# Kernel optimization log

Hardware: AMD Instinct MI355X
Metric: run time of the kernel (lower is better)

## Reference

```python
import jax, jax.numpy as jnp
import numpy as np

D_MODEL = 768
HEADS = 12
D_HEAD = D_MODEL // HEADS
D_DYNA = 768
EPS = 1e-5
B, SP, SI = 16, 256, 1024


def _layernorm(x, g, b):
    mu = jnp.mean(x, axis=-1, keepdims=True)
    var = jnp.var(x, axis=-1, keepdims=True)
    return (x - mu) * jax.lax.rsqrt(var + EPS) * g + b


def _mha(q, k, v, wq, bq, wk, bk, wv, bv, wo, bo):
    # weights stored [d_in, d_out]; torch Linear math y = x @ W^T + b is
    # equivalent with transposed storage.
    B_ = q.shape[0]
    qh = (q @ wq + bq).reshape(B_, -1, HEADS, D_HEAD)
    kh = (k @ wk + bk).reshape(B_, -1, HEADS, D_HEAD)
    vh = (v @ wv + bv).reshape(B_, -1, HEADS, D_HEAD)
    scores = jnp.einsum('bqhd,bkhd->bhqk', qh, kh) / np.sqrt(D_HEAD).astype(np.float32)
    attn = jax.nn.softmax(scores, axis=-1)  # dropout disabled (eval)
    out = jnp.einsum('bhqk,bkhd->bqhd', attn, vh).reshape(B_, -1, D_MODEL)
    return out @ wo + bo


def setup_inputs() -> dict:
    key = jax.random.key(0)
    ks = iter(jax.random.split(key, 40))
    s = 0.02
    d = {
        'image': jax.random.normal(next(ks), (B, SI, D_MODEL), jnp.float32),
        'prompt': jax.random.normal(next(ks), (B, SP, D_MODEL), jnp.float32),
        'posi': jax.random.normal(next(ks), (B, SI, D_MODEL), jnp.float32),
        'posp': jax.random.normal(next(ks), (B, SP, D_MODEL), jnp.float32),
    }
    for ln in ('ln_p1', 'ln_p2', 'ln_p3', 'ln_i1'):
        d[ln + '_g'] = jnp.ones((D_MODEL,), jnp.float32)
        d[ln + '_b'] = jnp.zeros((D_MODEL,), jnp.float32)
    for pre in ('pp', 'pi'):
        for nm in ('q', 'k', 'v', 'o'):
            d[f'{pre}_w{nm}'] = s * jax.random.normal(next(ks), (D_MODEL, D_MODEL), jnp.float32)
            d[f'{pre}_b{nm}'] = jnp.zeros((D_MODEL,), jnp.float32)
    d['ff_w1'] = s * jax.random.normal(next(ks), (D_MODEL, D_MODEL), jnp.float32)
    d['ff_b1'] = jnp.zeros((D_MODEL,), jnp.float32)
    d['ff_w2'] = s * jax.random.normal(next(ks), (D_MODEL, D_DYNA), jnp.float32)
    d['ff_b2'] = jnp.zeros((D_DYNA,), jnp.float32)
    return d


def reference(image, prompt, posi, posp,
              ln_p1_g, ln_p1_b, ln_p2_g, ln_p2_b, ln_p3_g, ln_p3_b, ln_i1_g, ln_i1_b,
              pp_wq, pp_bq, pp_wk, pp_bk, pp_wv, pp_bv, pp_wo, pp_bo,
              pi_wq, pi_bq, pi_wk, pi_bk, pi_wv, pi_bv, pi_wo, pi_bo,
              ff_w1, ff_b1, ff_w2, ff_b2):
    prompt0 = prompt + posp
    xp = _layernorm(prompt0, ln_p1_g, ln_p1_b)
    xp = _mha(xp, xp, xp, pp_wq, pp_bq, pp_wk, pp_bk, pp_wv, pp_bv, pp_wo, pp_bo)
    prompt = prompt + xp  # dropout_p1 is identity in eval
    xp = _layernorm(prompt + prompt0, ln_p2_g, ln_p2_b)
    xi = _layernorm(image + posi, ln_i1_g, ln_i1_b)
    xp = _mha(xp, xi, xi, pi_wq, pi_bq, pi_wk, pi_bk, pi_wv, pi_bv, pi_wo, pi_bo)
    prompt = prompt + xp  # dropout_p2 identity
    xp = _layernorm(prompt + prompt0, ln_p3_g, ln_p3_b)
    xp = jax.nn.relu(xp @ ff_w1 + ff_b1) @ ff_w2 + ff_b2
    return xp
```

## Files before the change

### kernel.cpp

```cpp
#include <hip/hip_runtime.h>
#include <hip/hip_bf16.h>
#include <stdint.h>
#include <math.h>

#define D_MODEL 768
#define HEADS 12
#define D_HEAD 64
#define BATCH 16
#define SP 256
#define SI 1024
#define NP (BATCH * SP)
#define NI (BATCH * SI)

#define GLOBAL_AS __attribute__((address_space(1)))
#define LDS_AS    __attribute__((address_space(3)))

typedef __attribute__((ext_vector_type(8))) short  frag_ab;
typedef __attribute__((ext_vector_type(4))) float  frag_cd;

static __device__ __forceinline__ ushort f2bf(float f) {
  __hip_bfloat16 h = __float2bfloat16(f);
  return *(ushort*)&h;
}
static __device__ __forceinline__ float bf2f(ushort u) {
  return __bfloat162float(*(__hip_bfloat16*)&u);
}
static __device__ __forceinline__ bool probe_bf(const uint32_t* p) {
  return p[0] == 0x3F803F80u;
}

struct Prep {
  const void* wsrc[10]; ushort* wdst[10];
  const void* vsrc[18]; float* vdst;
};

__global__ __launch_bounds__(256) void prep_kernel(Prep p, const uint32_t* probe) {
  const bool isbf = probe_bf(probe);
  const int z = blockIdx.z;
  if (z < 10) {
    __shared__ float tile[32][33];
    const int tx = threadIdx.x & 31, ty = threadIdx.x >> 5;
    const int x0 = blockIdx.x * 32, y0 = blockIdx.y * 32;
    const void* src = p.wsrc[z];
    ushort* dst = p.wdst[z];
#pragma unroll
    for (int i = 0; i < 4; i++) {
      const int y = y0 + ty + i * 8;
      float v;
      if (isbf) v = bf2f(((const ushort*)src)[(size_t)y * 768 + x0 + tx]);
      else      v = ((const float*)src)[(size_t)y * 768 + x0 + tx];
      tile[ty + i * 8][tx] = v;
    }
    __syncthreads();
#pragma unroll
    for (int i = 0; i < 4; i++) {
      const int row = x0 + ty + i * 8;
      const int col = y0 + tx;
      dst[(size_t)row * 768 + col] = f2bf(tile[tx][ty + i * 8]);
    }
  } else {
    const int idx = (blockIdx.y * 24 + blockIdx.x) * 256 + threadIdx.x;
    if (idx < 18 * 768) {
      const int e = idx / 768, i = idx - e * 768;
      float v;
      if (isbf) v = bf2f(((const ushort*)p.vsrc[e])[i]);
      else      v = ((const float*)p.vsrc[e])[i];
      p.vdst[idx] = v;
    }
  }
}

struct LNJob {
  const void* a; const void* b;
  const float* g; const float* be;
  float* sum_out; ushort* ln_out;
  int nrows; int abf;
};

__global__ __launch_bounds__(192) void add_ln2(LNJob J0, LNJob J1, const uint32_t* probe) {
  int row = blockIdx.x;
  LNJob j = (row < J0.nrows) ? J0 : J1;
  if (row >= J0.nrows) row -= J0.nrows;
  const int tid = threadIdx.x;
  const size_t base = (size_t)row * D_MODEL;
  const int c0 = tid * 4;
  const bool isbf = j.abf && probe_bf(probe);
  float x[4];
  if (isbf) {
    const uint2 ua = *(const uint2*)((const ushort*)j.a + base + c0);
    const uint2 ub = *(const uint2*)((const ushort*)j.b + base + c0);
    const ushort* pa = (const ushort*)&ua;
    const ushort* pb = (const ushort*)&ub;
#pragma unroll
    for (int t = 0; t < 4; t++) x[t] = bf2f(pa[t]) + bf2f(pb[t]);
  } else {
    const float4 fa = *(const float4*)((const float*)j.a + base + c0);
    const float4 fb = *(const float4*)((const float*)j.b + base + c0);
    x[0] = fa.x + fb.x; x[1] = fa.y + fb.y; x[2] = fa.z + fb.z; x[3] = fa.w + fb.w;
  }
  if (j.sum_out) {
    float4 s4; s4.x = x[0]; s4.y = x[1]; s4.z = x[2]; s4.w = x[3];
    *(float4*)&j.sum_out[base + c0] = s4;
  }
  __shared__ float rs[192], rq[192];
  __shared__ float stats[2];
  rs[tid] = x[0] + x[1] + x[2] + x[3];
  rq[tid] = x[0]*x[0] + x[1]*x[1] + x[2]*x[2] + x[3]*x[3];
  __syncthreads();
  if (tid < 64) {
    float s = rs[tid] + rs[tid + 64] + rs[tid + 128];
    float q = rq[tid] + rq[tid + 64] + rq[tid + 128];
#pragma unroll
    for (int o = 32; o > 0; o >>= 1) { s += __shfl_down(s, o); q += __shfl_down(q, o); }
    if (tid == 0) {
      const float mu  = s * (1.0f / D_MODEL);
      const float var = q * (1.0f / D_MODEL) - mu * mu;
      stats[0] = mu;
      stats[1] = rsqrtf(var + 1e-5f);
    }
  }
  __syncthreads();
  const float mu = stats[0], inv = stats[1];
  const float4 gv = *(const float4*)&j.g[c0];
  const float4 bv = *(const float4*)&j.be[c0];
  uint2 ou;
  ushort* oe = (ushort*)&ou;
  oe[0] = f2bf((x[0] - mu) * inv * gv.x + bv.x);
  oe[1] = f2bf((x[1] - mu) * inv * gv.y + bv.y);
  oe[2] = f2bf((x[2] - mu) * inv * gv.z + bv.z);
  oe[3] = f2bf((x[3] - mu) * inv * gv.w + bv.w);
  *(uint2*)(j.ln_out + base + c0) = ou;
}

#define BAR   __builtin_amdgcn_s_barrier()
#define LGKM0 do { asm volatile("s_waitcnt lgkmcnt(0)" ::: "memory"); \
                   __builtin_amdgcn_sched_barrier(0); } while (0)
#define VMC4  do { asm volatile("s_waitcnt vmcnt(4)" ::: "memory"); \
                   __builtin_amdgcn_sched_barrier(0); } while (0)

#define RD_A(SL) do { \
  const ushort* _b = &lds[SL][0][0]; \
  _Pragma("unroll") for (int _m = 0; _m < 4; ++_m) \
  _Pragma("unroll") for (int _k = 0; _k < 2; ++_k) \
    aF[_m][_k] = *(const frag_ab*)(_b + ((wr << 6) + _m * 16 + ml) * 64 + \
                                   (((_k << 5) + (kq << 3)) ^ swz)); \
} while (0)

#define RD_B(DST, SL, no) do { \
  const ushort* _b = &lds[SL][1][0]; \
  _Pragma("unroll") for (int _n = 0; _n < 2; ++_n) \
  _Pragma("unroll") for (int _k = 0; _k < 2; ++_k) \
    DST[_n][_k] = *(const frag_ab*)(_b + ((wc << 6) + (no) + _n * 16 + ml) * 64 + \
                                    (((_k << 5) + (kq << 3)) ^ swz)); \
} while (0)

#define MM(NB, BF) do { \
  __builtin_amdgcn_s_setprio(1); \
  _Pragma("unroll") for (int _m = 0; _m < 4; ++_m) \
  _Pragma("unroll") for (int _n = 0; _n < 2; ++_n) \
  _Pragma("unroll") for (int _k = 0; _k < 2; ++_k) \
    acc[_m][(NB) + _n] = __builtin_amdgcn_mfma_f32_16x16x32_bf16( \
        aF[_m][_k], BF[_n][_k], acc[_m][(NB) + _n], 0, 0, 0); \
  __builtin_amdgcn_s_setprio(0); \
} while (0)

#define STAGE(SL, RG, PTR, RBASE, KT) do { \
  const ushort* _p = (PTR) + (size_t)((RBASE) + srow) * 768 + ((KT) << 6) + scol; \
  _Pragma("unroll") for (int _j = 0; _j < 4; ++_j) \
    __builtin_amdgcn_global_load_lds( \
        (const GLOBAL_AS void*)(_p + (size_t)(_j * 32) * 768), \
        (LDS_AS void*)((LDS_AS ushort*)&lds[SL][RG][0] + (((_j << 2) + w) << 9)), \
        16, 0, 0); \
} while (0)

#define ENGINE128() do { \
  STAGE(0, 0, jA, m0, 0); \
  STAGE(0, 1, jB, n0, 0); \
  STAGE(1, 0, jA, m0, 1); \
  VMC4; BAR; \
  for (int it = 0; it < 6; ++it) { \
    const int t1  = 2 * it + 1; \
    const int tn0 = (2 * it + 2 < 12) ? 2 * it + 2 : 11; \
    const int tn1 = (2 * it + 3 < 12) ? 2 * it + 3 : 11; \
    RD_A(0); RD_B(bF0, 0, 0); \
    STAGE(1, 1, jB, n0, t1); \
    BAR; LGKM0; \
    MM(0, bF0); \
    BAR; \
    RD_B(bF1, 0, 32); \
    STAGE(0, 0, jA, m0, tn0); \
    BAR; LGKM0; \
    MM(2, bF1); \
    VMC4; BAR; \
    RD_A(1); RD_B(bF0, 1, 0); \
    STAGE(0, 1, jB, n0, tn0); \
    BAR; LGKM0; \
    MM(0, bF0); \
    BAR; \
    RD_B(bF1, 1, 32); \
    STAGE(1, 0, jA, m0, tn1); \
    BAR; LGKM0; \
    MM(2, bF1); \
    VMC4; BAR; \
  } \
} while (0)

struct GJob {
  const ushort* A; const ushort* Bt; const float* bias;
  ushort* o0; ushort* o1; ushort* vT;
  int X; int vsub; int shift;
};

__global__ __launch_bounds__(256, 2) void gemm_mega128(GJob J0, GJob J1, int n0blocks) {
  __shared__ __align__(16) ushort lds[2][2][8192];
  int bid = blockIdx.x;
  GJob j = (bid < n0blocks) ? J0 : J1;
  if (bid >= n0blocks) bid -= n0blocks;
  const int tid  = threadIdx.x;
  const int lane = tid & 63, w = tid >> 6;
  const int wr = w >> 1, wc = w & 1;
  const int ml = lane & 15, kq = lane >> 4;
  const int rest = bid >> 3;
  const int x = rest % j.X, y = (bid & 7) + 8 * (rest / j.X);
  const int m0 = y << 7, n0 = x << 7;
  const int srow = (w << 3) + (lane >> 3);
  const int scol = (((lane & 7) ^ (lane >> 3)) << 3);
  const int swz  = (ml & 7) << 3;
  const ushort* jA = j.A;
  const ushort* jB = j.Bt;

  frag_cd acc[4][4] = {};
  frag_ab aF[4][2], bF0[2][2], bF1[2][2];

  ENGINE128();

  const int sub  = x / 6;
  const int mask = (1 << j.shift) - 1;
#pragma unroll
  for (int mt = 0; mt < 4; mt++) {
#pragma unroll
    for (int nt = 0; nt < 4; nt++) {
      const int row0 = m0 + wr * 64 + mt * 16 + kq * 4;
      const int col  = n0 + wc * 64 + nt * 16 + ml;
      const float bc = j.bias[col];
      if (sub == j.vsub) {
        const int hcol = col - sub * 768;
        const int hh = hcol >> 6, dd = hcol & 63;
        const int bb = row0 >> j.shift;
        const int jj = row0 & mask;
        uint2 pack;
        ushort* pe = (ushort*)&pack;
#pragma unroll
        for (int r = 0; r < 4; r++) pe[r] = f2bf(acc[mt][nt][r] + bc);
        *(uint2*)(j.vT + ((((size_t)(bb * HEADS + hh) << 6) + dd) << j.shift) + jj) = pack;
      } else {
        ushort* out = (sub == 0) ? j.o0 : j.o1;
        const int cl = col - sub * 768;
#pragma unroll
        for (int r = 0; r < 4; r++)
          out[(size_t)(row0 + r) * 768 + cl] = f2bf(acc[mt][nt][r] + bc);
      }
    }
  }
}

__global__ __launch_bounds__(256, 2) void gemm_v3(
    const ushort* __restrict__ A, const ushort* __restrict__ Bt,
    const float* __restrict__ bias,
    const void* __restrict__ resid, int rmode,
    void* __restrict__ C, int relu, int omode,
    const uint32_t* __restrict__ probe, int X) {
  __shared__ __align__(16) ushort lds[2][2][8192];
  const int bid = blockIdx.x;
  const int tid  = threadIdx.x;
  const int lane = tid & 63, w = tid >> 6;
  const int wr = w >> 1, wc = w & 1;
  const int ml = lane & 15, kq = lane >> 4;
  const int rest = bid >> 3;
  const int x = rest % X, y = (bid & 7) + 8 * (rest / X);
  const int m0 = y << 7, n0 = x << 7;
  const int srow = (w << 3) + (lane >> 3);
  const int scol = (((lane & 7) ^ (lane >> 3)) << 3);
  const int swz  = (ml & 7) << 3;
  const ushort* jA = A;
  const ushort* jB = Bt;

  frag_cd acc[4][4] = {};
  frag_ab aF[4][2], bF0[2][2], bF1[2][2];

  ENGINE128();

  const bool obf = (omode == 1) || (omode == 2 && probe_bf(probe));
  const bool rbf = (rmode == 2) && probe_bf(probe);
#pragma unroll
  for (int mt = 0; mt < 4; mt++) {
#pragma unroll
    for (int nt = 0; nt < 4; nt++) {
      const int row0 = m0 + wr * 64 + mt * 16 + kq * 4;
      const int col  = n0 + wc * 64 + nt * 16 + ml;
      const float bc = bias[col];
#pragma unroll
      for (int r = 0; r < 4; r++) {
        const size_t off = (size_t)(row0 + r) * 768 + col;
        float v = acc[mt][nt][r] + bc;
        if (rmode != 0)
          v += rbf ? bf2f(((const ushort*)resid)[off]) : ((const float*)resid)[off];
        if (relu) v = fmaxf(v, 0.f);
        if (obf) ((ushort*)C)[off] = f2bf(v);
        else     ((float*)C)[off]  = v;
      }
    }
  }
}

#undef RD_A
#undef RD_B
#undef MM
#undef STAGE
#undef ENGINE128

#define FS 68
__global__ __launch_bounds__(256) void fattn_mfma(
    const ushort* __restrict__ Q, const ushort* __restrict__ Kp,
    const ushort* __restrict__ vT, ushort* __restrict__ O, int Skv) {
  __shared__ __align__(16) ushort Qs[64 * FS];
  __shared__ __align__(16) ushort Ks[64 * FS];
  __shared__ __align__(16) ushort Vt[64 * FS];
  __shared__ __align__(16) ushort Ps[64 * FS];
  const int tid  = threadIdx.x;
  const int lane = tid & 63, w = tid >> 6;
  const int ml   = lane & 15, kq = lane >> 4;
  const int bid = blockIdx.x;
  const int g8  = bid & 7;
  const int qt  = (bid >> 3) & 3;
  const int g   = (bid >> 5) * 8 + g8;
  const int h   = g % HEADS;
  const int b   = g / HEADS;
  const int q0  = qt * 64;
  const ushort* Qb  = Q  + ((size_t)b * SP + q0) * D_MODEL + h * D_HEAD;
  const ushort* Kb  = Kp + (size_t)b * Skv * D_MODEL + h * D_HEAD;
  const ushort* vTb = vT + (size_t)g * 64 * Skv;

  const int r0 = tid >> 3, p0 = tid & 7;
  const int r1 = r0 + 32;

  for (int c = tid; c < 512; c += 256) {
    const int r = c >> 3, p = c & 7;
    *(uint4*)&Qs[r * FS + p * 8] = *(const uint4*)(Qb + (size_t)r * D_MODEL + p * 8);
  }
  __syncthreads();
  frag_ab qa[2];
#pragma unroll
  for (int kc = 0; kc < 2; kc++)
    qa[kc] = *(const frag_ab*)&Qs[(w * 16 + ml) * FS + kc * 32 + kq * 8];

  frag_cd oc[4] = {};
  float m_i[4], l_i[4];
#pragma unroll
  for (int r = 0; r < 4; r++) { m_i[r] = -1e30f; l_i[r] = 0.f; }
  const float SCL = 0.125f * 1.44269504f;

  uint4 kr0 = *(const uint4*)(Kb + (size_t)r0 * D_MODEL + p0 * 8);
  uint4 vr0 = *(const uint4*)(vTb + (size_t)r0 * Skv + p0 * 8);
  uint4 kr1 = *(const uint4*)(Kb + (size_t)r1 * D_MODEL + p0 * 8);
  uint4 vr1 = *(const uint4*)(vTb + (size_t)r1 * Skv + p0 * 8);

  for (int j0 = 0; j0 < Skv; j0 += 64) {
    __syncthreads();
    *(uint4*)&Ks[r0 * FS + p0 * 8] = kr0;
    *(uint4*)&Vt[r0 * FS + p0 * 8] = vr0;
    *(uint4*)&Ks[r1 * FS + p0 * 8] = kr1;
    *(uint4*)&Vt[r1 * FS + p0 * 8] = vr1;
    __syncthreads();
    if (j0 + 64 < Skv) {
      const int jn = j0 + 64;
      kr0 = *(const uint4*)(Kb + (size_t)(jn + r0) * D_MODEL + p0 * 8);
      vr0 = *(const uint4*)(vTb + (size_t)r0 * Skv + jn + p0 * 8);
      kr1 = *(const uint4*)(Kb + (size_t)(jn + r1) * D_MODEL + p0 * 8);
      vr1 = *(const uint4*)(vTb + (size_t)r1 * Skv + jn + p0 * 8);
    }

    frag_cd sc[4] = {};
#pragma unroll
    for (int nt = 0; nt < 4; nt++)
#pragma unroll
      for (int kc = 0; kc < 2; kc++) {
        const frag_ab bfr = *(const frag_ab*)&Ks[(nt * 16 + ml) * FS + kc * 32 + kq * 8];
        sc[nt] = __builtin_amdgcn_mfma_f32_16x16x32_bf16(qa[kc], bfr, sc[nt], 0, 0, 0);
      }
#pragma unroll
    for (int nt = 0; nt < 4; nt++)
#pragma unroll
      for (int r = 0; r < 4; r++) sc[nt][r] *= SCL;

    float al[4];
#pragma unroll
    for (int r = 0; r < 4; r++) {
      float mx = fmaxf(fmaxf(sc[0][r], sc[1][r]), fmaxf(sc[2][r], sc[3][r]));
#pragma unroll
      for (int m = 1; m < 16; m <<= 1) mx = fmaxf(mx, __shfl_xor(mx, m, 16));
      const float mnew = fmaxf(m_i[r], mx);
      al[r] = exp2f(m_i[r] - mnew);
      float p[4], s = 0.f;
#pragma unroll
      for (int nt = 0; nt < 4; nt++) { p[nt] = exp2f(sc[nt][r] - mnew); s += p[nt]; }
#pragma unroll
      for (int m = 1; m < 16; m <<= 1) s += __shfl_xor(s, m, 16);
      l_i[r] = l_i[r] * al[r] + s;
      m_i[r] = mnew;
      const int prow = (w * 16 + kq * 4 + r) * FS;
#pragma unroll
      for (int nt = 0; nt < 4; nt++) Ps[prow + nt * 16 + ml] = f2bf(p[nt]);
    }
#pragma unroll
    for (int dt = 0; dt < 4; dt++)
#pragma unroll
      for (int r = 0; r < 4; r++) oc[dt][r] *= al[r];

#pragma unroll
    for (int kc = 0; kc < 2; kc++) {
      const frag_ab pa = *(const frag_ab*)&Ps[(w * 16 + ml) * FS + kc * 32 + kq * 8];
#pragma unroll
      for (int dt = 0; dt < 4; dt++) {
        const frag_ab vb = *(const frag_ab*)&Vt[(dt * 16 + ml) * FS + kc * 32 + kq * 8];
        oc[dt] = __builtin_amdgcn_mfma_f32_16x16x32_bf16(pa, vb, oc[dt], 0, 0, 0);
      }
    }
  }

  float inv[4];
#pragma unroll
  for (int r = 0; r < 4; r++) inv[r] = 1.0f / l_i[r];
#pragma unroll
  for (int dt = 0; dt < 4; dt++)
#pragma unroll
    for (int r = 0; r < 4; r++)
      O[((size_t)b * SP + q0 + w * 16 + kq * 4 + r) * D_MODEL + h * D_HEAD + dt * 16 + ml] =
          f2bf(oc[dt][r] * inv[r]);
}

extern "C" void kernel_launch(void* const* d_in, const int* in_sizes, int n_in,
                              void* d_out, int out_size, void* d_ws, size_t ws_size,
                              hipStream_t stream) {
  (void)in_sizes; (void)n_in; (void)out_size;
  char* base = (char*)d_ws;
  size_t off = 256;
  auto alloc = [&](size_t bytes) -> char* {
    char* p = base + off;
    off = (off + bytes + 255) & ~(size_t)255;
    return p;
  };
  const size_t WB = (size_t)768 * 768 * 2;
  ushort* Wt[10];
  for (int i = 0; i < 10; i++) Wt[i] = (ushort*)alloc(WB);
  float* vecs = (float*)alloc(18 * 768 * 4);
  float* biasF[10];
  for (int i = 0; i < 10; i++) biasF[i] = vecs + i * 768;
  float* lnF = vecs + 10 * 768;
  float* prompt0 = (float*)alloc((size_t)NP * 768 * 4);
  float* cur     = (float*)alloc((size_t)NP * 768 * 4);
  ushort* q_bf   = (ushort*)alloc((size_t)NP * 768 * 2);
  ushort* k_s    = (ushort*)alloc((size_t)NP * 768 * 2);
  ushort* k_c    = (ushort*)alloc((size_t)NI * 768 * 2);
  ushort* xln_bf = (ushort*)alloc((size_t)NP * 768 * 2);
  ushort* xi_bf  = (ushort*)alloc((size_t)NI * 768 * 2);
  ushort* obuf_bf = (ushort*)alloc((size_t)NP * 768 * 2);
  ushort* ffn1_bf = (ushort*)alloc((size_t)NP * 768 * 2);
  ushort* vT_s   = (ushort*)alloc((size_t)BATCH * HEADS * 64 * SP * 2);
  ushort* vT_c   = (ushort*)alloc((size_t)BATCH * HEADS * 64 * SI * 2);
  if (ws_size < off) return;

  const uint32_t* probe = (const uint32_t*)d_in[4];
  const int widx[10] = {12, 14, 16, 18, 20, 22, 24, 26, 28, 30};
  const int bidx[10] = {13, 15, 17, 19, 21, 23, 25, 27, 29, 31};

  Prep pr{};
  for (int i = 0; i < 10; i++) { pr.wsrc[i] = d_in[widx[i]]; pr.wdst[i] = Wt[i]; }
  for (int i = 0; i < 10; i++) pr.vsrc[i] = d_in[bidx[i]];
  for (int i = 0; i < 8;  i++) pr.vsrc[10 + i] = d_in[4 + i];
  pr.vdst = vecs;
  prep_kernel<<<dim3(24, 24, 11), 256, 0, stream>>>(pr, probe);

  float* G1 = lnF + 0 * 768, *B1 = lnF + 1 * 768;
  float* G2 = lnF + 2 * 768, *B2 = lnF + 3 * 768;
  float* G3 = lnF + 4 * 768, *B3 = lnF + 5 * 768;
  float* Gi = lnF + 6 * 768, *Bi = lnF + 7 * 768;

  LNJob L0{d_in[1], d_in[3], G1, B1, prompt0, xln_bf, NP, 1};
  LNJob Li{d_in[0], d_in[2], Gi, Bi, nullptr, xi_bf,  NI, 1};
  add_ln2<<<NP + NI, 192, 0, stream>>>(L0, Li, probe);

  GJob js{xln_bf, Wt[0], biasF[0], q_bf, k_s, vT_s, 18, 2, 8};
  GJob jc{xi_bf,  Wt[5], biasF[5], k_c,  nullptr, vT_c, 12, 1, 10};
  gemm_mega128<<<576 + 1536, 256, 0, stream>>>(js, jc, 576);

  fattn_mfma<<<BATCH * HEADS * (SP / 64), 256, 0, stream>>>(q_bf, k_s, vT_s, obuf_bf, SP);

  gemm_v3<<<192, 256, 0, stream>>>(obuf_bf, Wt[3], biasF[3],
      d_in[1], 2, cur, 0, 0, probe, 6);

  LNJob L2{cur, prompt0, G2, B2, nullptr, xln_bf, NP, 0};
  LNJob Lz{}; Lz.nrows = 0;
  add_ln2<<<NP, 192, 0, stream>>>(L2, Lz, probe);

  gemm_v3<<<192, 256, 0, stream>>>(xln_bf, Wt[4], biasF[4],
      nullptr, 0, q_bf, 0, 1, probe, 6);

  fattn_mfma<<<BATCH * HEADS * (SP / 64), 256, 0, stream>>>(q_bf, k_c, vT_c, obuf_bf, SI);

  gemm_v3<<<192, 256, 0, stream>>>(obuf_bf, Wt[7], biasF[7],
      cur, 1, cur, 0, 0, probe, 6);

  LNJob L3{cur, prompt0, G3, B3, nullptr, xln_bf, NP, 0};
  add_ln2<<<NP, 192, 0, stream>>>(L3, Lz, probe);

  gemm_v3<<<192, 256, 0, stream>>>(xln_bf, Wt[8], biasF[8],
      nullptr, 0, ffn1_bf, 1, 1, probe, 6);

  gemm_v3<<<192, 256, 0, stream>>>(ffn1_bf, Wt[9], biasF[9],
      nullptr, 0, d_out, 0, 2, probe, 6);
}
```

Baseline: 497.8 us.

## Double-buffer K/V tiles in flash attention and use wave-per-row layernorm

The attention kernel now keeps two LDS buffers for the K and V tiles. The next tile is stored into the idle buffer after the PV MFMAs, so each iteration needs one block barrier instead of two. This costs about double the K/V shared memory per block, which could lower occupancy. The add+layernorm kernel is also rewritten so one 64-lane wave handles a full 768-wide row with shuffle reductions, removing the shared-memory reduction and both __syncthreads, with four rows per 256-thread block.

```diff
diff --git a/kernel.cpp b/kernel.cpp
--- a/kernel.cpp
+++ b/kernel.cpp
@@ -77,59 +77,59 @@
   int nrows; int abf;
 };
 
-__global__ __launch_bounds__(192) void add_ln2(LNJob J0, LNJob J1, const uint32_t* probe) {
-  int row = blockIdx.x;
+__global__ __launch_bounds__(256) void add_ln_wave(LNJob J0, LNJob J1, const uint32_t* probe) {
+  const int w = threadIdx.x >> 6, lane = threadIdx.x & 63;
+  int row = blockIdx.x * 4 + w;
   LNJob j = (row < J0.nrows) ? J0 : J1;
   if (row >= J0.nrows) row -= J0.nrows;
-  const int tid = threadIdx.x;
+  if (row >= j.nrows) return;
   const size_t base = (size_t)row * D_MODEL;
-  const int c0 = tid * 4;
   const bool isbf = j.abf && probe_bf(probe);
-  float x[4];
-  if (isbf) {
-    const uint2 ua = *(const uint2*)((const ushort*)j.a + base + c0);
-    const uint2 ub = *(const uint2*)((const ushort*)j.b + base + c0);
-    const ushort* pa = (const ushort*)&ua;
-    const ushort* pb = (const ushort*)&ub;
-#pragma unroll
-    for (int t = 0; t < 4; t++) x[t] = bf2f(pa[t]) + bf2f(pb[t]);
-  } else {
-    const float4 fa = *(const float4*)((const float*)j.a + base + c0);
-    const float4 fb = *(const float4*)((const float*)j.b + base + c0);
-    x[0] = fa.x + fb.x; x[1] = fa.y + fb.y; x[2] = fa.z + fb.z; x[3] = fa.w + fb.w;
-  }
-  if (j.sum_out) {
-    float4 s4; s4.x = x[0]; s4.y = x[1]; s4.z = x[2]; s4.w = x[3];
-    *(float4*)&j.sum_out[base + c0] = s4;
-  }
-  __shared__ float rs[192], rq[192];
-  __shared__ float stats[2];
-  rs[tid] = x[0] + x[1] + x[2] + x[3];
-  rq[tid] = x[0]*x[0] + x[1]*x[1] + x[2]*x[2] + x[3]*x[3];
-  __syncthreads();
-  if (tid < 64) {
-    float s = rs[tid] + rs[tid + 64] + rs[tid + 128];
-    float q = rq[tid] + rq[tid + 64] + rq[tid + 128];
-#pragma unroll
-    for (int o = 32; o > 0; o >>= 1) { s += __shfl_down(s, o); q += __shfl_down(q, o); }
-    if (tid == 0) {
-      const float mu  = s * (1.0f / D_MODEL);
-      const float var = q * (1.0f / D_MODEL) - mu * mu;
-      stats[0] = mu;
-      stats[1] = rsqrtf(var + 1e-5f);
-    }
-  }
-  __syncthreads();
-  const float mu = stats[0], inv = stats[1];
-  const float4 gv = *(const float4*)&j.g[c0];
-  const float4 bv = *(const float4*)&j.be[c0];
-  uint2 ou;
-  ushort* oe = (ushort*)&ou;
-  oe[0] = f2bf((x[0] - mu) * inv * gv.x + bv.x);
-  oe[1] = f2bf((x[1] - mu) * inv * gv.y + bv.y);
-  oe[2] = f2bf((x[2] - mu) * inv * gv.z + bv.z);
-  oe[3] = f2bf((x[3] - mu) * inv * gv.w + bv.w);
-  *(uint2*)(j.ln_out + base + c0) = ou;
+  float x[12];
+#pragma unroll
+  for (int k = 0; k < 3; k++) {
+    const int c = k * 256 + lane * 4;
+    if (isbf) {
+      const uint2 ua = *(const uint2*)((const ushort*)j.a + base + c);
+      const uint2 ub = *(const uint2*)((const ushort*)j.b + base + c);
+      const ushort* pa = (const ushort*)&ua;
+      const ushort* pb = (const ushort*)&ub;
+#pragma unroll
+      for (int t = 0; t < 4; t++) x[k * 4 + t] = bf2f(pa[t]) + bf2f(pb[t]);
+    } else {
+      const float4 fa = *(const float4*)((const float*)j.a + base + c);
+      const float4 fb = *(const float4*)((const float*)j.b + base + c);
+      x[k * 4 + 0] = fa.x + fb.x; x[k * 4 + 1] = fa.y + fb.y;
+      x[k * 4 + 2] = fa.z + fb.z; x[k * 4 + 3] = fa.w + fb.w;
+    }
+    if (j.sum_out) {
+      float4 s4;
+      s4.x = x[k * 4 + 0]; s4.y = x[k * 4 + 1];
+      s4.z = x[k * 4 + 2]; s4.w = x[k * 4 + 3];
+      *(float4*)&j.sum_out[base + c] = s4;
+    }
+  }
+  float s = 0.f, q = 0.f;
+#pragma unroll
+  for (int t = 0; t < 12; t++) { s += x[t]; q += x[t] * x[t]; }
+#pragma unroll
+  for (int o = 32; o > 0; o >>= 1) { s += __shfl_xor(s, o); q += __shfl_xor(q, o); }
+  const float mu  = s * (1.0f / D_MODEL);
+  const float var = q * (1.0f / D_MODEL) - mu * mu;
+  const float inv = rsqrtf(var + 1e-5f);
+#pragma unroll
+  for (int k = 0; k < 3; k++) {
+    const int c = k * 256 + lane * 4;
+    const float4 gv = *(const float4*)&j.g[c];
+    const float4 bv = *(const float4*)&j.be[c];
+    uint2 ou;
+    ushort* oe = (ushort*)&ou;
+    oe[0] = f2bf((x[k * 4 + 0] - mu) * inv * gv.x + bv.x);
+    oe[1] = f2bf((x[k * 4 + 1] - mu) * inv * gv.y + bv.y);
+    oe[2] = f2bf((x[k * 4 + 2] - mu) * inv * gv.z + bv.z);
+    oe[3] = f2bf((x[k * 4 + 3] - mu) * inv * gv.w + bv.w);
+    *(uint2*)(j.ln_out + base + c) = ou;
+  }
 }
 
 #define BAR   __builtin_amdgcn_s_barrier()
@@ -324,8 +324,8 @@
     const ushort* __restrict__ Q, const ushort* __restrict__ Kp,
     const ushort* __restrict__ vT, ushort* __restrict__ O, int Skv) {
   __shared__ __align__(16) ushort Qs[64 * FS];
-  __shared__ __align__(16) ushort Ks[64 * FS];
-  __shared__ __align__(16) ushort Vt[64 * FS];
+  __shared__ __align__(16) ushort Ks[2][64 * FS];
+  __shared__ __align__(16) ushort Vt[2][64 * FS];
   __shared__ __align__(16) ushort Ps[64 * FS];
   const int tid  = threadIdx.x;
   const int lane = tid & 63, w = tid >> 6;
@@ -348,32 +348,33 @@
     const int r = c >> 3, p = c & 7;
     *(uint4*)&Qs[r * FS + p * 8] = *(const uint4*)(Qb + (size_t)r * D_MODEL + p * 8);
   }
-  __syncthreads();
-  frag_ab qa[2];
-#pragma unroll
-  for (int kc = 0; kc < 2; kc++)
-    qa[kc] = *(const frag_ab*)&Qs[(w * 16 + ml) * FS + kc * 32 + kq * 8];
-
-  frag_cd oc[4] = {};
-  float m_i[4], l_i[4];
-#pragma unroll
-  for (int r = 0; r < 4; r++) { m_i[r] = -1e30f; l_i[r] = 0.f; }
-  const float SCL = 0.125f * 1.44269504f;
 
   uint4 kr0 = *(const uint4*)(Kb + (size_t)r0 * D_MODEL + p0 * 8);
   uint4 vr0 = *(const uint4*)(vTb + (size_t)r0 * Skv + p0 * 8);
   uint4 kr1 = *(const uint4*)(Kb + (size_t)r1 * D_MODEL + p0 * 8);
   uint4 vr1 = *(const uint4*)(vTb + (size_t)r1 * Skv + p0 * 8);
-
-  for (int j0 = 0; j0 < Skv; j0 += 64) {
-    __syncthreads();
-    *(uint4*)&Ks[r0 * FS + p0 * 8] = kr0;
-    *(uint4*)&Vt[r0 * FS + p0 * 8] = vr0;
-    *(uint4*)&Ks[r1 * FS + p0 * 8] = kr1;
-    *(uint4*)&Vt[r1 * FS + p0 * 8] = vr1;
-    __syncthreads();
-    if (j0 + 64 < Skv) {
-      const int jn = j0 + 64;
+  *(uint4*)&Ks[0][r0 * FS + p0 * 8] = kr0;
+  *(uint4*)&Vt[0][r0 * FS + p0 * 8] = vr0;
+  *(uint4*)&Ks[0][r1 * FS + p0 * 8] = kr1;
+  *(uint4*)&Vt[0][r1 * FS + p0 * 8] = vr1;
+  __syncthreads();
+
+  frag_ab qa[2];
+#pragma unroll
+  for (int kc = 0; kc < 2; kc++)
+    qa[kc] = *(const frag_ab*)&Qs[(w * 16 + ml) * FS + kc * 32 + kq * 8];
+
+  frag_cd oc[4] = {};
+  float m_i[4], l_i[4];
+#pragma unroll
+  for (int r = 0; r < 4; r++) { m_i[r] = -1e30f; l_i[r] = 0.f; }
+  const float SCL = 0.125f * 1.44269504f;
+  const int NT = Skv >> 6;
+
+  for (int t = 0; t < NT; ++t) {
+    const int cb = t & 1;
+    if (t + 1 < NT) {
+      const int jn = (t + 1) << 6;
       kr0 = *(const uint4*)(Kb + (size_t)(jn + r0) * D_MODEL + p0 * 8);
       vr0 = *(const uint4*)(vTb + (size_t)r0 * Skv + jn + p0 * 8);
       kr1 = *(const uint4*)(Kb + (size_t)(jn + r1) * D_MODEL + p0 * 8);
@@ -385,7 +386,7 @@
     for (int nt = 0; nt < 4; nt++)
 #pragma unroll
       for (int kc = 0; kc < 2; kc++) {
-        const frag_ab bfr = *(const frag_ab*)&Ks[(nt * 16 + ml) * FS + kc * 32 + kq * 8];
+        const frag_ab bfr = *(const frag_ab*)&Ks[cb][(nt * 16 + ml) * FS + kc * 32 + kq * 8];
         sc[nt] = __builtin_amdgcn_mfma_f32_16x16x32_bf16(qa[kc], bfr, sc[nt], 0, 0, 0);
       }
 #pragma unroll
@@ -422,9 +423,17 @@
       const frag_ab pa = *(const frag_ab*)&Ps[(w * 16 + ml) * FS + kc * 32 + kq * 8];
 #pragma unroll
       for (int dt = 0; dt < 4; dt++) {
-        const frag_ab vb = *(const frag_ab*)&Vt[(dt * 16 + ml) * FS + kc * 32 + kq * 8];
+        const frag_ab vb = *(const frag_ab*)&Vt[cb][(dt * 16 + ml) * FS + kc * 32 + kq * 8];
         oc[dt] = __builtin_amdgcn_mfma_f32_16x16x32_bf16(pa, vb, oc[dt], 0, 0, 0);
       }
+    }
+
+    if (t + 1 < NT) {
+      *(uint4*)&Ks[cb ^ 1][r0 * FS + p0 * 8] = kr0;
+      *(uint4*)&Vt[cb ^ 1][r0 * FS + p0 * 8] = vr0;
+      *(uint4*)&Ks[cb ^ 1][r1 * FS + p0 * 8] = kr1;
+      *(uint4*)&Vt[cb ^ 1][r1 * FS + p0 * 8] = vr1;
+      __syncthreads();
     }
   }
 
@@ -488,7 +497,7 @@
 
   LNJob L0{d_in[1], d_in[3], G1, B1, prompt0, xln_bf, NP, 1};
   LNJob Li{d_in[0], d_in[2], Gi, Bi, nullptr, xi_bf,  NI, 1};
-  add_ln2<<<NP + NI, 192, 0, stream>>>(L0, Li, probe);
+  add_ln_wave<<<(NP + NI) / 4, 256, 0, stream>>>(L0, Li, probe);
 
   GJob js{xln_bf, Wt[0], biasF[0], q_bf, k_s, vT_s, 18, 2, 8};
   GJob jc{xi_bf,  Wt[5], biasF[5], k_c,  nullptr, vT_c, 12, 1, 10};
@@ -501,7 +510,7 @@
 
   LNJob L2{cur, prompt0, G2, B2, nullptr, xln_bf, NP, 0};
   LNJob Lz{}; Lz.nrows = 0;
-  add_ln2<<<NP, 192, 0, stream>>>(L2, Lz, probe);
+  add_ln_wave<<<NP / 4, 256, 0, stream>>>(L2, Lz, probe);
 
   gemm_v3<<<192, 256, 0, stream>>>(xln_bf, Wt[4], biasF[4],
       nullptr, 0, q_bf, 0, 1, probe, 6);
@@ -512,7 +521,7 @@
       cur, 1, cur, 0, 0, probe, 6);
 
   LNJob L3{cur, prompt0, G3, B3, nullptr, xln_bf, NP, 0};
-  add_ln2<<<NP, 192, 0, stream>>>(L3, Lz, probe);
+  add_ln_wave<<<NP / 4, 256, 0, stream>>>(L3, Lz, probe);
 
   gemm_v3<<<192, 256, 0, stream>>>(xln_bf, Wt[8], biasF[8],
       nullptr, 0, ffn1_bf, 1, 1, probe, 6);
```

Result: no change. 490.3 us (-1.5%).
